# Performance work log

Hardware: AMD Instinct MI355X
Metric: run time of the kernel (lower is better)

Reference implementation:

```python
import jax, jax.numpy as jnp
import numpy as np

D_IN = 1024
D_OUT = 1024


def setup_inputs() -> dict:
    key = jax.random.key(0)
    kx, kq, kk, kv = jax.random.split(key, 4)
    x = jax.random.normal(kx, (4, 2048, D_IN), dtype=jnp.float32)
    s = 1.0 / np.sqrt(D_IN)
    Wq = jax.random.normal(kq, (D_IN, D_OUT), dtype=jnp.float32) * s
    Wk = jax.random.normal(kk, (D_IN, D_OUT), dtype=jnp.float32) * s
    Wv = jax.random.normal(kv, (D_IN, D_OUT), dtype=jnp.float32) * s
    return {"x": x, "Wq": Wq, "Wk": Wk, "Wv": Wv}


def reference(x, Wq, Wk, Wv):
    # x: [b, s, d_in]; projections [b, s, d_out]
    q = jnp.einsum('bsd,de->bse', x, Wq)
    k = jnp.einsum('bsd,de->bse', x, Wk)
    v = jnp.einsum('bsd,de->bse', x, Wv)
    scale = 1.0 / jnp.sqrt(jnp.asarray(D_OUT, dtype=x.dtype))
    scores = jnp.einsum('bqe,bke->bqk', q, k) * scale  # [b, s, s]
    s_len = x.shape[1]
    causal = jnp.tril(jnp.ones((s_len, s_len), dtype=bool))
    scores = jnp.where(causal[None, :, :], scores, -jnp.inf)
    attn = jax.nn.softmax(scores, axis=-1)
    # dropout p=0.0 -> identity
    return jnp.einsum('bqk,bke->bqe', attn, v)
```

## Files before the change

### kernel.cpp

```cpp
#include <hip/hip_runtime.h>
#include <hip/hip_bf16.h>

#define S_LEN 2048
#define D_DIM 1024
#define NBATCH 4

typedef __attribute__((ext_vector_type(4)))  float f32x4;
typedef __attribute__((ext_vector_type(8)))  short s16x8;
typedef __attribute__((ext_vector_type(4)))  unsigned short u16x4;

__device__ __forceinline__ unsigned short f2b(float f) {
    __hip_bfloat16 h = __float2bfloat16(f);
    return __builtin_bit_cast(unsigned short, h);
}

__device__ __forceinline__ void load_lds16(const unsigned short* g, unsigned short* l) {
    __builtin_amdgcn_global_load_lds(
        (const __attribute__((address_space(1))) void*)(g),
        (__attribute__((address_space(3))) void*)(l), 16, 0, 0);
}

__global__ __launch_bounds__(256)
void cvt_kernel(const float* __restrict__ in, unsigned short* __restrict__ out) {
    long i = ((long)blockIdx.x * 256 + threadIdx.x) * 4;
    f32x4 v = *(const f32x4*)(in + i);
    u16x4 o;
    o.x = f2b(v.x); o.y = f2b(v.y); o.z = f2b(v.z); o.w = f2b(v.w);
    *(u16x4*)(out + i) = o;
}

__global__ __launch_bounds__(256)
void transW_kernel(const float* __restrict__ W0, const float* __restrict__ W1,
                   const float* __restrict__ W2, unsigned short* __restrict__ WT) {
    const float* W = (blockIdx.z == 0) ? W0 : (blockIdx.z == 1) ? W1 : W2;
    unsigned short* O = WT + (long)blockIdx.z * 1024 * 1024;
    __shared__ float t[32][33];
    int tid = threadIdx.x;
    int r  = tid >> 3;
    int c4 = tid & 7;
    int bi = blockIdx.x, bj = blockIdx.y;
    f32x4 v = *(const f32x4*)&W[(long)(bi * 32 + r) * 1024 + bj * 32 + c4 * 4];
    t[r][c4 * 4 + 0] = v.x; t[r][c4 * 4 + 1] = v.y;
    t[r][c4 * 4 + 2] = v.z; t[r][c4 * 4 + 3] = v.w;
    __syncthreads();
    u16x4 o;
    o.x = f2b(t[c4 * 4 + 0][r]); o.y = f2b(t[c4 * 4 + 1][r]);
    o.z = f2b(t[c4 * 4 + 2][r]); o.w = f2b(t[c4 * 4 + 3][r]);
    *(u16x4*)&O[(long)(bj * 32 + r) * 1024 + bi * 32 + c4 * 4] = o;
}

template<int OMODE, bool CSKIP, bool CKLIM>
__global__ __launch_bounds__(512, 2)
void gemm_cnt(const unsigned short* __restrict__ A, int lda, long aStride,
              const unsigned short* __restrict__ Bt, int ldb, long bStride,
              void* __restrict__ Cv, int ldc, long cStride,
              int K, float alpha) {
    constexpr int BUF = (128 + 256) * 64;
    const int bm = (CSKIP || CKLIM) ? (gridDim.x - 1 - blockIdx.x) : blockIdx.x;
    const int bn = blockIdx.y, bz = blockIdx.z;
    if (CSKIP && 2 * bn > bm) return;
    A  += (long)bz * aStride;
    Bt += (long)bz * bStride;

    const int tid  = threadIdx.x;
    const int lane = tid & 63;
    const int wid  = tid >> 6;
    const int wm   = wid >> 2;
    const int wn   = wid & 3;

    extern __shared__ __align__(16) unsigned short smem[];

    f32x4 acc[4][4] = {};

    const int kend = CKLIM ? (bm + 1) * 128 : K;
    const int nt   = kend / 64;

    const int srl = tid >> 3;
    const int sg  = (tid & 7) ^ (srl & 7);
    const unsigned short* agb = A  + (long)(bm * 128 + srl) * lda + sg * 8;
    const unsigned short* bgb = Bt + (long)(bn * 256 + srl) * ldb + sg * 8;

    const int fr   = lane & 15;
    const int fg   = lane >> 4;
    const int rxor = (fr & 7) * 8;

    auto stage = [&](int t) {
        const int k0 = t * 64;
        unsigned short* d = smem + (t % 3) * BUF;
        #pragma unroll
        for (int i = 0; i < 2; ++i)
            load_lds16(agb + (long)(i * 64) * lda + k0, d + i * 4096 + tid * 8);
        #pragma unroll
        for (int i = 0; i < 4; ++i)
            load_lds16(bgb + (long)(i * 64) * ldb + k0, d + 8192 + i * 4096 + tid * 8);
    };

    stage(0);
    stage(1);

    for (int t = 0; t < nt; ++t) {
        if (t + 1 < nt) asm volatile("s_waitcnt vmcnt(6)" ::: "memory");
        else            asm volatile("s_waitcnt vmcnt(0)" ::: "memory");
        __builtin_amdgcn_s_barrier();
        if (t + 2 < nt) stage(t + 2);

        const unsigned short* as = smem + (t % 3) * BUF;
        const unsigned short* bs = as + 8192;
        #pragma unroll
        for (int ks = 0; ks < 2; ++ks) {
            s16x8 af[4], bf[4];
            #pragma unroll
            for (int m = 0; m < 4; ++m) {
                const int row = wm * 64 + m * 16 + fr;
                af[m] = *(const s16x8*)&as[row * 64 + (((ks * 4 + fg) * 8) ^ rxor)];
            }
            #pragma unroll
            for (int n = 0; n < 4; ++n) {
                const int row = wn * 64 + n * 16 + fr;
                bf[n] = *(const s16x8*)&bs[row * 64 + (((ks * 4 + fg) * 8) ^ rxor)];
            }
            __builtin_amdgcn_s_setprio(1);
            #pragma unroll
            for (int m = 0; m < 4; ++m)
                #pragma unroll
                for (int n = 0; n < 4; ++n)
                    acc[m][n] = __builtin_amdgcn_mfma_f32_16x16x32_bf16(af[m], bf[n], acc[m][n], 0, 0, 0);
            __builtin_amdgcn_s_setprio(0);
        }
    }

    const int crow0 = bm * 128 + wm * 64;
    const int ccol0 = bn * 256 + wn * 64;
    const int cr = (lane >> 4) * 4;
    const int cc = lane & 15;
    if (OMODE == 0) {
        unsigned short* C = (unsigned short*)Cv + (long)bz * cStride;
        #pragma unroll
        for (int m = 0; m < 4; ++m)
            #pragma unroll
            for (int r = 0; r < 4; ++r) {
                const long row = crow0 + m * 16 + cr + r;
                #pragma unroll
                for (int n = 0; n < 4; ++n)
                    C[row * ldc + ccol0 + n * 16 + cc] = f2b(acc[m][n][r] * alpha);
            }
    } else {
        float* C = (float*)Cv + (long)bz * cStride;
        #pragma unroll
        for (int m = 0; m < 4; ++m)
            #pragma unroll
            for (int r = 0; r < 4; ++r) {
                const long row = crow0 + m * 16 + cr + r;
                #pragma unroll
                for (int n = 0; n < 4; ++n)
                    C[row * ldc + ccol0 + n * 16 + cc] = acc[m][n][r] * alpha;
            }
    }
}

__global__ __launch_bounds__(256)
void softmax_rows(float* __restrict__ scores) {
    const int i = blockIdx.x;
    const int z = blockIdx.y;
    float* row = scores + ((long)z * S_LEN + i) * S_LEN;
    const int c = i + 1;
    const int tid  = threadIdx.x;
    const int lane = tid & 63;
    const int wid  = tid >> 6;

    f32x4 v0 = ((const f32x4*)row)[tid];
    f32x4 v1 = ((const f32x4*)row)[tid + 256];
    const int j0 = tid * 4, j1 = (tid + 256) * 4;

    float m = -3.4e38f;
    #pragma unroll
    for (int e = 0; e < 4; e++) {
        if (j0 + e < c) m = fmaxf(m, v0[e]);
        if (j1 + e < c) m = fmaxf(m, v1[e]);
    }
    #pragma unroll
    for (int off = 32; off > 0; off >>= 1) m = fmaxf(m, __shfl_xor(m, off));
    __shared__ float redm[4];
    if (lane == 0) redm[wid] = m;
    __syncthreads();
    m = fmaxf(fmaxf(redm[0], redm[1]), fmaxf(redm[2], redm[3]));

    float e0[4], e1[4];
    float s = 0.f;
    #pragma unroll
    for (int e = 0; e < 4; e++) {
        e0[e] = (j0 + e < c) ? __expf(v0[e] - m) : 0.f;
        e1[e] = (j1 + e < c) ? __expf(v1[e] - m) : 0.f;
        s += e0[e] + e1[e];
    }
    #pragma unroll
    for (int off = 32; off > 0; off >>= 1) s += __shfl_xor(s, off);
    __shared__ float reds[4];
    if (lane == 0) reds[wid] = s;
    __syncthreads();
    s = reds[0] + reds[1] + reds[2] + reds[3];
    const float rinv = 1.f / s;

    unsigned short* P = (unsigned short*)row;
    u16x4 o0, o1;
    o0.x = f2b(e0[0] * rinv); o0.y = f2b(e0[1] * rinv);
    o0.z = f2b(e0[2] * rinv); o0.w = f2b(e0[3] * rinv);
    o1.x = f2b(e1[0] * rinv); o1.y = f2b(e1[1] * rinv);
    o1.z = f2b(e1[2] * rinv); o1.w = f2b(e1[3] * rinv);
    *(u16x4*)&P[j0] = o0;
    *(u16x4*)&P[j1] = o1;
}

extern "C" void kernel_launch(void* const* d_in, const int* in_sizes, int n_in,
                              void* d_out, int out_size, void* d_ws, size_t ws_size,
                              hipStream_t stream) {
    const float* x  = (const float*)d_in[0];
    const float* Wq = (const float*)d_in[1];
    const float* Wk = (const float*)d_in[2];
    const float* Wv = (const float*)d_in[3];
    float* out = (float*)d_out;
    char* ws = (char*)d_ws;
    const size_t MiB = 1ull << 20;

    unsigned short* xb  = (unsigned short*)(ws);
    unsigned short* WT  = (unsigned short*)(ws + 16 * MiB);
    unsigned short* Qb  = (unsigned short*)(ws + 22 * MiB);
    unsigned short* Kb  = (unsigned short*)(ws + 38 * MiB);
    unsigned short* VbT = (unsigned short*)(ws + 54 * MiB);
    float* scores       = (float*)(ws + 70 * MiB);

    int nb;
    if      (ws_size >= (70 + 64) * MiB) nb = 4;
    else if (ws_size >= (70 + 32) * MiB) nb = 2;
    else                                 nb = 1;

    const int LDS = 3 * (128 + 256) * 64 * 2;
    hipFuncSetAttribute((const void*)gemm_cnt<0,false,false>,
                        hipFuncAttributeMaxDynamicSharedMemorySize, LDS);
    hipFuncSetAttribute((const void*)gemm_cnt<1,true,false>,
                        hipFuncAttributeMaxDynamicSharedMemorySize, LDS);
    hipFuncSetAttribute((const void*)gemm_cnt<1,false,true>,
                        hipFuncAttributeMaxDynamicSharedMemorySize, LDS);

    cvt_kernel<<<8192, 256, 0, stream>>>(x, xb);
    transW_kernel<<<dim3(32, 32, 3), 256, 0, stream>>>(Wq, Wk, Wv, WT);

    gemm_cnt<0,false,false><<<dim3(64, 4, 2), 512, LDS, stream>>>(
        xb, 1024, 0L, WT, 1024, (long)1024 * 1024,
        Qb, 1024, (long)8192 * 1024, 1024, 1.0f);
    gemm_cnt<0,false,false><<<dim3(8, 32, 1), 512, LDS, stream>>>(
        WT + (long)2 * 1024 * 1024, 1024, 0L, xb, 1024, 0L,
        VbT, 8192, 0L, 1024, 1.0f);

    const float alpha = 0.03125f;
    for (int b0 = 0; b0 < NBATCH; b0 += nb) {
        const int nz = (NBATCH - b0 < nb) ? (NBATCH - b0) : nb;
        gemm_cnt<1,true,false><<<dim3(16, 8, nz), 512, LDS, stream>>>(
            Qb + (long)b0 * S_LEN * D_DIM, 1024, (long)S_LEN * D_DIM,
            Kb + (long)b0 * S_LEN * D_DIM, 1024, (long)S_LEN * D_DIM,
            scores, S_LEN, (long)S_LEN * S_LEN, 1024, alpha);
        softmax_rows<<<dim3(S_LEN, nz), 256, 0, stream>>>(scores);
        gemm_cnt<1,false,true><<<dim3(16, 4, nz), 512, LDS, stream>>>(
            (const unsigned short*)scores, 2 * S_LEN, 2L * S_LEN * S_LEN,
            VbT + (long)b0 * S_LEN, 8192, (long)S_LEN,
            out + (long)b0 * S_LEN * D_DIM, 1024, (long)S_LEN * D_DIM,
            S_LEN, 1.0f);
    }
}
```

Measured before the change: 245.9 us.

## Use 256x256 GEMM tiles with K=32 stages and split-K for causal PV

The main GEMM now uses 256x256 output tiles with 32-wide K stages, a new swizzled LDS layout and an 8x4 MFMA accumulator per wave, which raises arithmetic intensity per tile. The causal QK^T skip is adapted to the larger tiles. The PV GEMM for the upper half of rows is split along K into two partial products, with an extra add kernel summing them, to balance the triangular workload. The V-transposed projection keeps the old tile shape in a separate kernel. The changes add register pressure from 128 accumulators, a partial buffer that reuses workspace, and an extra launch.

Result: no change. 247.3 us (+0.6%).

```diff
diff --git a/kernel.cpp b/kernel.cpp
--- a/kernel.cpp
+++ b/kernel.cpp
@@ -49,16 +49,21 @@
     *(u16x4*)&O[(long)(bj * 32 + r) * 1024 + bi * 32 + c4 * 4] = o;
 }
 
-template<int OMODE, bool CSKIP, bool CKLIM>
+template<int OMODE, bool CSKIP, bool KRANGE>
 __global__ __launch_bounds__(512, 2)
-void gemm_cnt(const unsigned short* __restrict__ A, int lda, long aStride,
-              const unsigned short* __restrict__ Bt, int ldb, long bStride,
-              void* __restrict__ Cv, int ldc, long cStride,
-              int K, float alpha) {
-    constexpr int BUF = (128 + 256) * 64;
-    const int bm = (CSKIP || CKLIM) ? (gridDim.x - 1 - blockIdx.x) : blockIdx.x;
+void gemm_A(const unsigned short* __restrict__ A, int lda, long aStride,
+            const unsigned short* __restrict__ Bt, int ldb, long bStride,
+            void* __restrict__ Cv, int ldc, long cStride,
+            int K, float alpha, float* __restrict__ pv2, int nlo, int kcap) {
+    constexpr int BUF = 16384;
+    int bm = blockIdx.x;
     const int bn = blockIdx.y, bz = blockIdx.z;
-    if (CSKIP && 2 * bn > bm) return;
+    if (CSKIP && bn > bm) return;
+    int kbeg = 0, kend = K;
+    if (KRANGE) {
+        if (bm < nlo) { kend = min((bm + 1) * 256, kcap); }
+        else          { bm = bm - nlo + (kcap >> 8); kbeg = kcap; kend = (bm + 1) * 256; }
+    }
     A  += (long)bz * aStride;
     Bt += (long)bz * bStride;
 
@@ -70,73 +75,70 @@
 
     extern __shared__ __align__(16) unsigned short smem[];
 
-    f32x4 acc[4][4] = {};
-
-    const int kend = CKLIM ? (bm + 1) * 128 : K;
-    const int nt   = kend / 64;
-
-    const int srl = tid >> 3;
-    const int sg  = (tid & 7) ^ (srl & 7);
-    const unsigned short* agb = A  + (long)(bm * 128 + srl) * lda + sg * 8;
-    const unsigned short* bgb = Bt + (long)(bn * 256 + srl) * ldb + sg * 8;
-
-    const int fr   = lane & 15;
-    const int fg   = lane >> 4;
-    const int rxor = (fr & 7) * 8;
+    f32x4 acc[8][4] = {};
+    const int nt = (kend - kbeg) >> 5;
+
+    const int giA0 = tid, giA1 = 512 + tid;
+    auto src = [&](const unsigned short* base, int ld, int rbase, int gi) {
+        const int line = gi >> 3, u = (gi & 7) ^ (line & 7);
+        return base + (long)(rbase + line * 2 + (u >> 2)) * ld + (u & 3) * 8;
+    };
+    const unsigned short* pa0 = src(A,  lda, bm * 256, giA0);
+    const unsigned short* pa1 = src(A,  lda, bm * 256, giA1);
+    const unsigned short* pb0 = src(Bt, ldb, bn * 256, giA0);
+    const unsigned short* pb1 = src(Bt, ldb, bn * 256, giA1);
+    const int dst0 = giA0 * 8, dst1 = giA1 * 8;
+
+    const int fr  = lane & 15;
+    const int fg  = lane >> 4;
+    const int fr2 = fr >> 1;
+    const int g8r = (((fr & 1) << 2) | fg) ^ fr2;
+    const int loff = fr2 * 64 + g8r * 8;
 
     auto stage = [&](int t) {
-        const int k0 = t * 64;
+        const int k0 = kbeg + t * 32;
         unsigned short* d = smem + (t % 3) * BUF;
-        #pragma unroll
-        for (int i = 0; i < 2; ++i)
-            load_lds16(agb + (long)(i * 64) * lda + k0, d + i * 4096 + tid * 8);
-        #pragma unroll
-        for (int i = 0; i < 4; ++i)
-            load_lds16(bgb + (long)(i * 64) * ldb + k0, d + 8192 + i * 4096 + tid * 8);
+        load_lds16(pa0 + k0, d + dst0);
+        load_lds16(pa1 + k0, d + dst1);
+        load_lds16(pb0 + k0, d + 8192 + dst0);
+        load_lds16(pb1 + k0, d + 8192 + dst1);
     };
 
     stage(0);
     stage(1);
 
     for (int t = 0; t < nt; ++t) {
-        if (t + 1 < nt) asm volatile("s_waitcnt vmcnt(6)" ::: "memory");
+        if (t + 1 < nt) asm volatile("s_waitcnt vmcnt(4)" ::: "memory");
         else            asm volatile("s_waitcnt vmcnt(0)" ::: "memory");
         __builtin_amdgcn_s_barrier();
         if (t + 2 < nt) stage(t + 2);
 
         const unsigned short* as = smem + (t % 3) * BUF;
         const unsigned short* bs = as + 8192;
-        #pragma unroll
-        for (int ks = 0; ks < 2; ++ks) {
-            s16x8 af[4], bf[4];
-            #pragma unroll
-            for (int m = 0; m < 4; ++m) {
-                const int row = wm * 64 + m * 16 + fr;
-                af[m] = *(const s16x8*)&as[row * 64 + (((ks * 4 + fg) * 8) ^ rxor)];
-            }
-            #pragma unroll
-            for (int n = 0; n < 4; ++n) {
-                const int row = wn * 64 + n * 16 + fr;
-                bf[n] = *(const s16x8*)&bs[row * 64 + (((ks * 4 + fg) * 8) ^ rxor)];
-            }
-            __builtin_amdgcn_s_setprio(1);
-            #pragma unroll
-            for (int m = 0; m < 4; ++m)
-                #pragma unroll
-                for (int n = 0; n < 4; ++n)
-                    acc[m][n] = __builtin_amdgcn_mfma_f32_16x16x32_bf16(af[m], bf[n], acc[m][n], 0, 0, 0);
-            __builtin_amdgcn_s_setprio(0);
-        }
-    }
-
-    const int crow0 = bm * 128 + wm * 64;
+        s16x8 af[8], bf[4];
+        #pragma unroll
+        for (int m = 0; m < 8; ++m)
+            af[m] = *(const s16x8*)&as[(wm * 64 + m * 8) * 64 + loff];
+        #pragma unroll
+        for (int n = 0; n < 4; ++n)
+            bf[n] = *(const s16x8*)&bs[(wn * 32 + n * 8) * 64 + loff];
+        __builtin_amdgcn_s_setprio(1);
+        #pragma unroll
+        for (int m = 0; m < 8; ++m)
+            #pragma unroll
+            for (int n = 0; n < 4; ++n)
+                acc[m][n] = __builtin_amdgcn_mfma_f32_16x16x32_bf16(af[m], bf[n], acc[m][n], 0, 0, 0);
+        __builtin_amdgcn_s_setprio(0);
+    }
+
+    const int crow0 = bm * 256 + wm * 128;
     const int ccol0 = bn * 256 + wn * 64;
     const int cr = (lane >> 4) * 4;
     const int cc = lane & 15;
     if (OMODE == 0) {
         unsigned short* C = (unsigned short*)Cv + (long)bz * cStride;
         #pragma unroll
-        for (int m = 0; m < 4; ++m)
+        for (int m = 0; m < 8; ++m)
             #pragma unroll
             for (int r = 0; r < 4; ++r) {
                 const long row = crow0 + m * 16 + cr + r;
@@ -145,9 +147,10 @@
                     C[row * ldc + ccol0 + n * 16 + cc] = f2b(acc[m][n][r] * alpha);
             }
     } else {
-        float* C = (float*)Cv + (long)bz * cStride;
-        #pragma unroll
-        for (int m = 0; m < 4; ++m)
+        float* C = (KRANGE && blockIdx.x >= nlo) ? (pv2 + (long)bz * cStride)
+                                                 : ((float*)Cv + (long)bz * cStride);
+        #pragma unroll
+        for (int m = 0; m < 8; ++m)
             #pragma unroll
             for (int r = 0; r < 4; ++r) {
                 const long row = crow0 + m * 16 + cr + r;
@@ -156,6 +159,87 @@
                     C[row * ldc + ccol0 + n * 16 + cc] = acc[m][n][r] * alpha;
             }
     }
+}
+
+__global__ __launch_bounds__(512, 2)
+void gemm_B(const unsigned short* __restrict__ A, int lda,
+            const unsigned short* __restrict__ Bt, int ldb,
+            unsigned short* __restrict__ C, int ldc, int K) {
+    constexpr int BUF = (128 + 256) * 64;
+    const int bm = blockIdx.x, bn = blockIdx.y;
+    const int tid  = threadIdx.x;
+    const int lane = tid & 63;
+    const int wid  = tid >> 6;
+    const int wm   = wid >> 2;
+    const int wn   = wid & 3;
+
+    extern __shared__ __align__(16) unsigned short smem[];
+    f32x4 acc[4][4] = {};
+    const int nt = K / 64;
+
+    const int srl = tid >> 3;
+    const int sg  = (tid & 7) ^ (srl & 7);
+    const unsigned short* agb = A  + (long)(bm * 128 + srl) * lda + sg * 8;
+    const unsigned short* bgb = Bt + (long)(bn * 256 + srl) * ldb + sg * 8;
+
+    const int fr   = lane & 15;
+    const int fg   = lane >> 4;
+    const int rxor = (fr & 7) * 8;
+
+    auto stage = [&](int t) {
+        const int k0 = t * 64;
+        unsigned short* d = smem + (t % 3) * BUF;
+        #pragma unroll
+        for (int i = 0; i < 2; ++i)
+            load_lds16(agb + (long)(i * 64) * lda + k0, d + i * 4096 + tid * 8);
+        #pragma unroll
+        for (int i = 0; i < 4; ++i)
+            load_lds16(bgb + (long)(i * 64) * ldb + k0, d + 8192 + i * 4096 + tid * 8);
+    };
+
+    stage(0);
+    stage(1);
+
+    for (int t = 0; t < nt; ++t) {
+        if (t + 1 < nt) asm volatile("s_waitcnt vmcnt(6)" ::: "memory");
+        else            asm volatile("s_waitcnt vmcnt(0)" ::: "memory");
+        __builtin_amdgcn_s_barrier();
+        if (t + 2 < nt) stage(t + 2);
+
+        const unsigned short* as = smem + (t % 3) * BUF;
+        const unsigned short* bs = as + 8192;
+        #pragma unroll
+        for (int ks = 0; ks < 2; ++ks) {
+            s16x8 af[4], bf[4];
+            #pragma unroll
+            for (int m = 0; m < 4; ++m)
+                af[m] = *(const s16x8*)&as[(wm * 64 + m * 16 + fr) * 64 + (((ks * 4 + fg) * 8) ^ rxor)];
+            #pragma unroll
+            for (int n = 0; n < 4; ++n)
+                bf[n] = *(const s16x8*)&bs[(wn * 64 + n * 16 + fr) * 64 + (((ks * 4 + fg) * 8) ^ rxor)];
+            __builtin_amdgcn_s_setprio(1);
+            #pragma unroll
+            for (int m = 0; m < 4; ++m)
+                #pragma unroll
+                for (int n = 0; n < 4; ++n)
+                    acc[m][n] = __builtin_amdgcn_mfma_f32_16x16x32_bf16(af[m], bf[n], acc[m][n], 0, 0, 0);
+            __builtin_amdgcn_s_setprio(0);
+        }
+    }
+
+    const int crow0 = bm * 128 + wm * 64;
+    const int ccol0 = bn * 256 + wn * 64;
+    const int cr = (lane >> 4) * 4;
+    const int cc = lane & 15;
+    #pragma unroll
+    for (int m = 0; m < 4; ++m)
+        #pragma unroll
+        for (int r = 0; r < 4; ++r) {
+            const long row = crow0 + m * 16 + cr + r;
+            #pragma unroll
+            for (int n = 0; n < 4; ++n)
+                C[row * ldc + ccol0 + n * 16 + cc] = f2b(acc[m][n][r]);
+        }
 }
 
 __global__ __launch_bounds__(256)
@@ -209,6 +293,18 @@
     o1.z = f2b(e1[2] * rinv); o1.w = f2b(e1[3] * rinv);
     *(u16x4*)&P[j0] = o0;
     *(u16x4*)&P[j1] = o1;
+}
+
+__global__ __launch_bounds__(256)
+void add_upper(float* __restrict__ out, const float* __restrict__ pv2) {
+    const long gi = (long)blockIdx.x * 256 + threadIdx.x;
+    const long z = gi >> 18;
+    const long r = gi & 262143;
+    const long idx = z * 2097152 + 1048576 + r * 4;
+    f32x4 a = *(const f32x4*)(out + idx);
+    f32x4 b = *(const f32x4*)(pv2 + idx);
+    a.x += b.x; a.y += b.y; a.z += b.z; a.w += b.w;
+    *(f32x4*)(out + idx) = a;
 }
 
 extern "C" void kernel_launch(void* const* d_in, const int* in_sizes, int n_in,
@@ -228,42 +324,55 @@
     unsigned short* Kb  = (unsigned short*)(ws + 38 * MiB);
     unsigned short* VbT = (unsigned short*)(ws + 54 * MiB);
     float* scores       = (float*)(ws + 70 * MiB);
+    float* pv2          = (float*)(ws);
 
     int nb;
     if      (ws_size >= (70 + 64) * MiB) nb = 4;
     else if (ws_size >= (70 + 32) * MiB) nb = 2;
     else                                 nb = 1;
-
-    const int LDS = 3 * (128 + 256) * 64 * 2;
-    hipFuncSetAttribute((const void*)gemm_cnt<0,false,false>,
-                        hipFuncAttributeMaxDynamicSharedMemorySize, LDS);
-    hipFuncSetAttribute((const void*)gemm_cnt<1,true,false>,
-                        hipFuncAttributeMaxDynamicSharedMemorySize, LDS);
-    hipFuncSetAttribute((const void*)gemm_cnt<1,false,true>,
-                        hipFuncAttributeMaxDynamicSharedMemorySize, LDS);
+    const bool splitK = (nb == 4);
+
+    const int LDSA = 3 * 16384 * 2;
+    const int LDSB = 3 * (128 + 256) * 64 * 2;
+    hipFuncSetAttribute((const void*)gemm_A<0,false,false>,
+                        hipFuncAttributeMaxDynamicSharedMemorySize, LDSA);
+    hipFuncSetAttribute((const void*)gemm_A<1,true,false>,
+                        hipFuncAttributeMaxDynamicSharedMemorySize, LDSA);
+    hipFuncSetAttribute((const void*)gemm_A<1,false,true>,
+                        hipFuncAttributeMaxDynamicSharedMemorySize, LDSA);
+    hipFuncSetAttribute((const void*)gemm_B,
+                        hipFuncAttributeMaxDynamicSharedMemorySize, LDSB);
 
     cvt_kernel<<<8192, 256, 0, stream>>>(x, xb);
     transW_kernel<<<dim3(32, 32, 3), 256, 0, stream>>>(Wq, Wk, Wv, WT);
 
-    gemm_cnt<0,false,false><<<dim3(64, 4, 2), 512, LDS, stream>>>(
+    gemm_A<0,false,false><<<dim3(32, 4, 2), 512, LDSA, stream>>>(
         xb, 1024, 0L, WT, 1024, (long)1024 * 1024,
-        Qb, 1024, (long)8192 * 1024, 1024, 1.0f);
-    gemm_cnt<0,false,false><<<dim3(8, 32, 1), 512, LDS, stream>>>(
-        WT + (long)2 * 1024 * 1024, 1024, 0L, xb, 1024, 0L,
-        VbT, 8192, 0L, 1024, 1.0f);
+        Qb, 1024, (long)8192 * 1024, 1024, 1.0f, nullptr, 0, 0);
+    gemm_B<<<dim3(8, 32), 512, LDSB, stream>>>(
+        WT + (long)2 * 1024 * 1024, 1024, xb, 1024, VbT, 8192, 1024);
 
     const float alpha = 0.03125f;
     for (int b0 = 0; b0 < NBATCH; b0 += nb) {
         const int nz = (NBATCH - b0 < nb) ? (NBATCH - b0) : nb;
-        gemm_cnt<1,true,false><<<dim3(16, 8, nz), 512, LDS, stream>>>(
+        gemm_A<1,true,false><<<dim3(8, 8, nz), 512, LDSA, stream>>>(
             Qb + (long)b0 * S_LEN * D_DIM, 1024, (long)S_LEN * D_DIM,
             Kb + (long)b0 * S_LEN * D_DIM, 1024, (long)S_LEN * D_DIM,
-            scores, S_LEN, (long)S_LEN * S_LEN, 1024, alpha);
+            scores, S_LEN, (long)S_LEN * S_LEN, 1024, alpha, nullptr, 0, 0);
         softmax_rows<<<dim3(S_LEN, nz), 256, 0, stream>>>(scores);
-        gemm_cnt<1,false,true><<<dim3(16, 4, nz), 512, LDS, stream>>>(
-            (const unsigned short*)scores, 2 * S_LEN, 2L * S_LEN * S_LEN,
-            VbT + (long)b0 * S_LEN, 8192, (long)S_LEN,
-            out + (long)b0 * S_LEN * D_DIM, 1024, (long)S_LEN * D_DIM,
-            S_LEN, 1.0f);
-    }
-}
+        if (splitK) {
+            gemm_A<1,false,true><<<dim3(12, 4, nz), 512, LDSA, stream>>>(
+                (const unsigned short*)scores, 2 * S_LEN, 2L * S_LEN * S_LEN,
+                VbT + (long)b0 * S_LEN, 8192, (long)S_LEN,
+                out + (long)b0 * S_LEN * D_DIM, 1024, (long)S_LEN * D_DIM,
+                2048, 1.0f, pv2, 8, 1024);
+            add_upper<<<4096, 256, 0, stream>>>(out, pv2);
+        } else {
+            gemm_A<1,false,true><<<dim3(8, 4, nz), 512, LDSA, stream>>>(
+                (const unsigned short*)scores, 2 * S_LEN, 2L * S_LEN * S_LEN,
+                VbT + (long)b0 * S_LEN, 8192, (long)S_LEN,
+                out + (long)b0 * S_LEN * D_DIM, 1024, (long)S_LEN * D_DIM,
+                2048, 1.0f, nullptr, 8, 1 << 30);
+        }
+    }
+}
```
